# Optimization experiments

Hardware: AMD Instinct MI355X
Metric: run time of the kernel (lower is better)

## Reference

```python
import jax, jax.numpy as jnp
import numpy as np

D_MODEL = 192
NODE_NUM = 64
DEPTH = 2
ALPHA = 0.05
NUM_LAYERS = 2
LN_EPS = 1e-5


def _gcn(x, p):
    # x: [N, in_dim*D_MODEL]; faithful port of GCN.forward (eval mode)
    nv1, nv2, ws, bs, wm, bm, we, be, wl, bl, g, b = p
    N = x.shape[0]
    in_dim = x.shape[1] // D_MODEL
    adp = jax.nn.softmax(jax.nn.relu(nv1 @ nv2), axis=1)            # [V,V]
    adj = adp + jnp.eye(NODE_NUM, dtype=x.dtype)
    a = adj / adj.sum(1, keepdims=True)                              # row-normalized
    h0 = jax.lax.conv_general_dilated(
        x.reshape(N, in_dim, D_MODEL), ws, (1,), 'VALID',
        dimension_numbers=('NCH', 'OIH', 'NCH')) + bs[None, :, None]  # [N,C,V]
    h = h0
    outs = [h0]
    for _ in range(DEPTH):
        h = ALPHA * h0 + (1.0 - ALPHA) * jnp.einsum('ncw,vw->ncv', h, a)
        outs.append(h)
    ho = jnp.concatenate(outs, axis=1)                               # [N,(DEPTH+1)C,V]
    ho = jax.nn.gelu(jnp.einsum('ncv,oc->nov', ho, wm) + bm[None, :, None], approximate=False)
    ho = jnp.einsum('ncv,oc->nov', ho, we) + be[None, :, None]       # [N,6,V]
    ho = jnp.einsum('nov,dv->nod', ho, wl) + bl                      # [N,6,D]
    mu = ho.mean(-1, keepdims=True)
    var = ((ho - mu) ** 2).mean(-1, keepdims=True)                   # biased, like torch LN
    ho = (ho - mu) / jnp.sqrt(var + LN_EPS) * g + b
    return ho.reshape(N, 6 * D_MODEL)


def _encoder(inp4, flag, layer_params):
    x = jnp.transpose(inp4, (2, 0, 1, 3)) if flag == 1 else jnp.transpose(inp4, (1, 0, 2, 3))
    W, B, O, D = x.shape
    L = W + O - 1
    N = W * B
    # input_transfer: shift row r by r along the slice axis
    place = jax.vmap(lambda xr, r: jax.lax.dynamic_update_slice(
        jnp.zeros((B, L, D), x.dtype), xr, (0, r, 0)))
    a = place(x, jnp.arange(W)).reshape(N, L, D)
    layer0_output = None
    output_all = None
    rows_layers, cols_layers = [], []
    for layer in range(NUM_LAYERS):
        if layer >= 1:
            a = output_all  # eval mode: F.dropout is identity
            if layer == 1:
                layer0_output = a
        p = layer_params[layer]

        def step(carry, x_t, p=p):
            h_row, h_col = carry
            gate = _gcn(jnp.concatenate([h_row, h_col, x_t], axis=-1), p)  # [N,6D]
            sg = jax.nn.sigmoid(gate[:, :4 * D])
            tg = jnp.tanh(gate[:, 4 * D:])
            ug_r, og_r, ug_c, og_c = jnp.split(sg, 4, axis=-1)
            ig_r, ig_c = jnp.split(tg, 2, axis=-1)
            h_row = jnp.tanh((1.0 - ug_r) * h_row + ug_r * ig_r) * og_r
            h_col = jnp.tanh((1.0 - ug_c) * h_col + ug_c * ig_c) * og_c
            out_s = jnp.concatenate([h_row, h_col], axis=-1)
            # col hidden is saved pre-roll, rolled for next step
            return (h_row, jnp.roll(h_col, B, axis=0)), (out_s, h_row, h_col)

        init = (jnp.zeros((N, D), x.dtype), jnp.zeros((N, D), x.dtype))
        _, (outs, hrows, hcols) = jax.lax.scan(step, init, jnp.swapaxes(a, 0, 1))
        output_all = jnp.swapaxes(outs, 0, 1)                        # [N,L,2D]
        if layer >= 1:
            output_all = output_all + layer0_output
        # rows saved at slice s>=O-1 from block loc = s-O+1
        rows = hrows.reshape(L, W, B, D)[jnp.arange(O - 1, L), jnp.arange(W)]  # [W,B,D]
        # cols saved at slice s>=W-1 from last batch block
        cols = hcols[W - 1:, (W - 1) * B:, :]                        # [O,B,D]
        rows_layers.append(rows)
        cols_layers.append(cols)
    hidden_row_all = jnp.stack(rows_layers).transpose(2, 0, 1, 3)    # [B,layers,W,D]
    hidden_col_all = jnp.stack(cols_layers).transpose(2, 0, 1, 3)    # [B,layers,O,D]
    if flag == 1:
        return output_all, hidden_col_all, hidden_row_all
    return output_all, hidden_row_all, hidden_col_all


def setup_inputs() -> dict:
    key = jax.random.key(0)
    ks = jax.random.split(key, 20)
    idx = [0]
    def nxt():
        k = ks[idx[0]]
        idx[0] += 1
        return k
    B, W, O = 8, 24, 48
    K = D_MODEL - NODE_NUM + 1  # 129
    cc, sc, nd = 16, 32, 40
    d = {"input": jax.random.normal(nxt(), (B, W, O, D_MODEL), dtype=jnp.float32)}
    for li, in_dim in enumerate([3, 4]):
        d[f"nodevec1_{li}"] = jax.random.normal(nxt(), (NODE_NUM, nd), dtype=jnp.float32)
        d[f"nodevec2_{li}"] = jax.random.normal(nxt(), (nd, NODE_NUM), dtype=jnp.float32)
        d[f"w_start_{li}"] = jax.random.normal(nxt(), (cc, in_dim, K), dtype=jnp.float32) * 0.05
        d[f"b_start_{li}"] = jnp.zeros((cc,), jnp.float32)
        d[f"w_mlp_{li}"] = jax.random.normal(nxt(), (sc, (DEPTH + 1) * cc), dtype=jnp.float32) * 0.05
        d[f"b_mlp_{li}"] = jnp.zeros((sc,), jnp.float32)
        d[f"w_end_{li}"] = jax.random.normal(nxt(), (6, sc), dtype=jnp.float32) * 0.05
        d[f"b_end_{li}"] = jnp.zeros((6,), jnp.float32)
        d[f"w_lin_{li}"] = jax.random.normal(nxt(), (D_MODEL, NODE_NUM), dtype=jnp.float32) * 0.05
        d[f"b_lin_{li}"] = jnp.zeros((D_MODEL,), jnp.float32)
        d[f"gamma_{li}"] = jnp.ones((D_MODEL,), jnp.float32)
        d[f"beta_{li}"] = jnp.zeros((D_MODEL,), jnp.float32)
    d["flag"] = 0
    return d


def reference(input, nodevec1_0, nodevec2_0, w_start_0, b_start_0, w_mlp_0, b_mlp_0,
              w_end_0, b_end_0, w_lin_0, b_lin_0, gamma_0, beta_0,
              nodevec1_1, nodevec2_1, w_start_1, b_start_1, w_mlp_1, b_mlp_1,
              w_end_1, b_end_1, w_lin_1, b_lin_1, gamma_1, beta_1, flag):
    p0 = (nodevec1_0, nodevec2_0, w_start_0, b_start_0, w_mlp_0, b_mlp_0,
          w_end_0, b_end_0, w_lin_0, b_lin_0, gamma_0, beta_0)
    p1 = (nodevec1_1, nodevec2_1, w_start_1, b_start_1, w_mlp_1, b_mlp_1,
          w_end_1, b_end_1, w_lin_1, b_lin_1, gamma_1, beta_1)
    return _encoder(input, flag, (p0, p1))
```

## Files before the change

### kernel.cpp

```cpp
#include <hip/hip_runtime.h>
#include <hip/hip_bf16.h>

#define NT 512
typedef unsigned short u16;
typedef unsigned long long u64;

__device__ __forceinline__ u16 tobf(float x) {
  union { __hip_bfloat16 h; u16 u; } cv;
  cv.h = __float2bfloat16(x);
  return cv.u;
}
__device__ __forceinline__ float frombf(u16 u) {
  return __uint_as_float(((unsigned)u) << 16);
}
__device__ __forceinline__ float sigf(float x) {
  return __builtin_amdgcn_rcpf(1.f + __builtin_amdgcn_exp2f(-1.4426950408889634f * x));
}
__device__ __forceinline__ float tanh_fast(float x) {
  return 1.f - 2.f * __builtin_amdgcn_rcpf(1.f + __builtin_amdgcn_exp2f(2.8853900817779268f * x));
}
__device__ __forceinline__ void lds_fence() {
  asm volatile("s_waitcnt lgkmcnt(0)" ::: "memory");
  __builtin_amdgcn_sched_barrier(0);
}
__device__ __forceinline__ void bar_light() {
  asm volatile("s_waitcnt lgkmcnt(0)" ::: "memory");
  __builtin_amdgcn_s_barrier();
  asm volatile("" ::: "memory");
}

struct SeqArgs {
  const float* input;
  const float* nv1_0; const float* nv2_0; const float* nv1_1; const float* nv2_1;
  const float* w_start0; const float* b_start0; const float* w_mlp0; const float* b_mlp0;
  const float* w_end0;   const float* b_end0;   const float* w_lin0; const float* b_lin0;
  const float* gamma0;   const float* beta0;
  const float* w_start1; const float* b_start1; const float* w_mlp1; const float* b_mlp1;
  const float* w_end1;   const float* b_end1;   const float* w_lin1; const float* b_lin1;
  const float* gamma1;   const float* beta1;
  u64*   HCOL2;
  int*   prog;
  float* out_all; float* out_hrow; float* out_hcol;
};

__global__ __launch_bounds__(NT, 2) void seq_kernel(SeqArgs A) {
  const int n = blockIdx.x, w = n >> 3, b = n & 7, tid = threadIdx.x;
  const int pred = (n + 184) % 192;
  const int succ = (n + 8) % 192;

  __shared__ __align__(16) float sCIN[768];
  __shared__ __align__(16) u16   sWS[64 * 132];
  __shared__ __align__(16) float sAT[4096];
  __shared__ __align__(16) float sH[2][1024];
  __shared__ __align__(16) float sAbuf[4928];
  float* const sPart = sAbuf;
  float* const sG    = sAbuf;
  float* const sH2c  = sAbuf + 2048;
  float* const sE    = sAbuf + 2048;
  float* const sY    = sAbuf;
  float* const smWE  = sAbuf + 3072;
  float* const smBE  = sAbuf + 3264;
  float* const smWM  = sAbuf + 3328;

  for (int layer = 0; layer < 2; ++layer) {
    const int in_dim = 3 + layer;
    const int P = in_dim - 1;
    const float* nv1    = layer ? A.nv1_1    : A.nv1_0;
    const float* nv2    = layer ? A.nv2_1    : A.nv2_0;
    const float* wstart = layer ? A.w_start1 : A.w_start0;
    const float* bs     = layer ? A.b_start1 : A.b_start0;
    const float* wm     = layer ? A.w_mlp1   : A.w_mlp0;
    const float* bm     = layer ? A.b_mlp1   : A.b_mlp0;
    const float* we     = layer ? A.w_end1   : A.w_end0;
    const float* be     = layer ? A.b_end1   : A.b_end0;
    const float* wl     = layer ? A.w_lin1   : A.w_lin0;
    const float* bl     = layer ? A.b_lin1   : A.b_lin0;
    const float* gm     = layer ? A.gamma1   : A.gamma0;
    const float* bt     = layer ? A.beta1    : A.beta0;

    for (int idx = tid; idx < 4096; idx += NT) {
      int v = idx >> 6, ww = idx & 63;
      float s = 0.f;
      for (int j = 0; j < 40; ++j) s = fmaf(nv1[v*40 + j], nv2[j*64 + ww], s);
      sAbuf[idx] = fmaxf(s, 0.f);
    }
    __syncthreads();
    if (tid < 64) {
      const int v = tid;
      float m = -1e30f;
      for (int ww = 0; ww < 64; ++ww) m = fmaxf(m, sAbuf[v*64 + ww]);
      float s = 0.f;
      for (int ww = 0; ww < 64; ++ww) { float e = expf(sAbuf[v*64 + ww] - m); sAbuf[v*64 + ww] = e; s += e; }
      float inv = 1.f / s, rs = 1.f;
      for (int ww = 0; ww < 64; ++ww) rs += sAbuf[v*64 + ww] * inv;
      float irs = 1.f / rs;
      for (int ww = 0; ww < 64; ++ww) {
        float a = sAbuf[v*64 + ww] * inv + ((ww == v) ? 1.f : 0.f);
        sAT[ww*64 + v] = a * irs;
      }
    }
    __syncthreads();
    for (int idx = tid; idx < 16*in_dim*132; idx += NT) {
      int row = idx / 132, k = idx - row*132;
      sWS[idx] = (k < 129) ? tobf(wstart[((row & 15)*in_dim + (row >> 4))*129 + k]) : (u16)0;
    }
    for (int idx = tid; idx < 1536; idx += NT) { int o = idx/48, c = idx - o*48; smWM[o*50 + c] = wm[idx]; }
    for (int idx = tid; idx < 192; idx += NT) smWE[idx] = we[idx];
    if (tid < 6) smBE[tid] = be[tid];
    for (int d = tid; d < 384; d += NT) sCIN[d] = 0.f;

    const int v_p = tid & 63;
    const int o0  = tid >> 6;
    const float bmv0 = bm[o0], bmv1 = bm[o0 + 8], bmv2 = bm[o0 + 16], bmv3 = bm[o0 + 24];
    float blv = 0.f, gmv = 1.f, btv = 0.f;
    if (tid < 384) blv = bl[(tid >= 192) ? tid - 192 : tid];
    if (tid < 192) { gmv = gm[tid]; btv = bt[tid]; }
    float bs_r[2];
    bs_r[0] = bs[tid >> 6];
    bs_r[1] = bs[(tid >> 6) + 8];
    __syncthreads();

    auto pre_conv = [&]() {
      const int nslots = P << 8;
      for (int s = tid; s < nslots; s += NT) {
        const int cidx = s >> 4;
        const int p = cidx >> 4, c = cidx & 15;
        const int vg = s & 15;
        const int ich = (p == 0) ? 0 : (p + 1);
        const float* xin = ((p == 0) ? &sCIN[0] : &sCIN[384 + (p-1)*192]) + vg*4;
        const u16* wrow = &sWS[(ich*16 + c)*132];
        float a0 = 0.f, a1 = 0.f, a2 = 0.f, a3 = 0.f;
        float4 xc = *(const float4*)xin;
        for (int k4 = 0; k4 < 128; k4 += 4) {
          ushort4 wu = *(const ushort4*)(wrow + k4);
          float w0 = frombf(wu.x), w1 = frombf(wu.y), w2 = frombf(wu.z), w3 = frombf(wu.w);
          float4 xn = *(const float4*)(xin + k4 + 4);
          a0 = fmaf(w3, xc.w, fmaf(w2, xc.z, fmaf(w1, xc.y, fmaf(w0, xc.x, a0))));
          a1 = fmaf(w3, xn.x, fmaf(w2, xc.w, fmaf(w1, xc.z, fmaf(w0, xc.y, a1))));
          a2 = fmaf(w3, xn.y, fmaf(w2, xn.x, fmaf(w1, xc.w, fmaf(w0, xc.z, a2))));
          a3 = fmaf(w3, xn.z, fmaf(w2, xn.y, fmaf(w1, xn.x, fmaf(w0, xc.w, a3))));
          xc = xn;
        }
        float wk = frombf(wrow[128]);
        a0 = fmaf(wk, xc.x, a0); a1 = fmaf(wk, xc.y, a1);
        a2 = fmaf(wk, xc.z, a2); a3 = fmaf(wk, xc.w, a3);
        *(float4*)&sPart[cidx*64 + vg*4] = make_float4(a0, a1, a2, a3);
      }
      bar_light();
      {
        const int c0 = tid >> 6, v = tid & 63;
        float sum0 = bs_r[0], sum1 = bs_r[1];
        for (int p = 0; p < P; ++p) {
          sum0 += sPart[(p*16 + c0     )*64 + v];
          sum1 += sPart[(p*16 + c0 + 8 )*64 + v];
        }
        sH[0][ c0      *64 + v] = sum0;
        sH[0][(c0 + 8 )*64 + v] = sum1;
      }
      bar_light();
    };

    {
      if (layer == 0) {
        int o = 0 - w;
        if (o >= 0 && o < 48) {
          const float* xr = A.input + (((size_t)(b*24 + w)*48 + o)*192);
          for (int d = tid; d < 192; d += NT) sCIN[384 + d] = xr[d];
        } else {
          for (int d = tid; d < 192; d += NT) sCIN[384 + d] = 0.f;
        }
      } else {
        const float* xr = A.out_all + ((size_t)n*71 + 0)*384;
        for (int d = tid; d < 384; d += NT) sCIN[384 + d] = xr[d];
      }
      bar_light();
      pre_conv();
    }

    for (int t = 0; t < 71; ++t) {
      const int S = layer*71 + t;

      float xpa = 0.f, xpb = 0.f;
      if (t < 70 && tid < 192) {
        if (layer == 0) {
          int o = (t + 1) - w;
          if (o >= 0 && o < 48)
            xpa = A.input[(((size_t)(b*24 + w)*48 + o)*192) + tid];
        } else {
          const float* xr = A.out_all + ((size_t)n*71 + (t+1))*384;
          xpa = xr[tid];
          xpb = xr[192 + tid];
        }
      }

      if (t > 0) {
        if (tid < 192) {
          const u64* src = &A.HCOL2[((size_t)((S-1) & 15)*192 + pred)*192 + tid];
          u64 v;
          do {
            v = __hip_atomic_load(src, __ATOMIC_RELAXED, __HIP_MEMORY_SCOPE_AGENT);
          } while ((unsigned)(v >> 32) != (unsigned)S);
          sCIN[192 + tid] = __uint_as_float((unsigned)v);
        } else if (tid == 256 && S >= 16) {
          while (__hip_atomic_load(&A.prog[succ*32], __ATOMIC_RELAXED, __HIP_MEMORY_SCOPE_AGENT) < S - 15)
            __builtin_amdgcn_s_sleep(2);
        }
        bar_light();
        if (tid == 0)
          __hip_atomic_store(&A.prog[n*32], S, __ATOMIC_RELAXED, __HIP_MEMORY_SCOPE_AGENT);
      } else if (S >= 16) {
        if (tid == 256) {
          while (__hip_atomic_load(&A.prog[succ*32], __ATOMIC_RELAXED, __HIP_MEMORY_SCOPE_AGENT) < S - 15)
            __builtin_amdgcn_s_sleep(2);
        }
      }

      {
        const int c = tid >> 5, vg2 = tid & 31;
        const int vbase = c*64 + vg2*2;
        const float* xin = &sCIN[192 + vg2*2];
        const u16* wrow = &sWS[(16 + c)*132];
        float a0 = sH[0][vbase], a1 = sH[0][vbase + 1];
        float2 xc = *(const float2*)xin;
        for (int k2 = 0; k2 < 128; k2 += 2) {
          ushort2 wu = *(const ushort2*)(wrow + k2);
          float w0 = frombf(wu.x), w1 = frombf(wu.y);
          float2 xn = *(const float2*)(xin + k2 + 2);
          a0 = fmaf(w1, xc.y, fmaf(w0, xc.x, a0));
          a1 = fmaf(w1, xn.x, fmaf(w0, xc.y, a1));
          xc = xn;
        }
        float wk = frombf(wrow[128]);
        a0 = fmaf(wk, xc.x, a0); a1 = fmaf(wk, xc.y, a1);
        sH[0][vbase] = a0; sH[0][vbase + 1] = a1;
      }
      lds_fence();
      {
        const int c0 = o0 * 2;
        float pa0 = 0.f, pa1 = 0.f;
        for (int w4 = 0; w4 < 64; w4 += 4) {
          float a0v = sAT[(w4+0)*64 + v_p];
          float a1v = sAT[(w4+1)*64 + v_p];
          float a2v = sAT[(w4+2)*64 + v_p];
          float a3v = sAT[(w4+3)*64 + v_p];
          float4 h0v = *(const float4*)&sH[0][ c0      *64 + w4];
          float4 h1v = *(const float4*)&sH[0][(c0 + 1 )*64 + w4];
          pa0 = fmaf(h0v.x, a0v, pa0); pa0 = fmaf(h0v.y, a1v, pa0);
          pa0 = fmaf(h0v.z, a2v, pa0); pa0 = fmaf(h0v.w, a3v, pa0);
          pa1 = fmaf(h1v.x, a0v, pa1); pa1 = fmaf(h1v.y, a1v, pa1);
          pa1 = fmaf(h1v.z, a2v, pa1); pa1 = fmaf(h1v.w, a3v, pa1);
        }
        float h0a = sH[0][ c0      *64 + v_p];
        float h0b = sH[0][(c0 + 1 )*64 + v_p];
        sH[1][ c0      *64 + v_p] = fmaf(0.95f, pa0, 0.05f * h0a);
        sH[1][(c0 + 1 )*64 + v_p] = fmaf(0.95f, pa1, 0.05f * h0b);
        lds_fence();
        float pb0 = 0.f, pb1 = 0.f;
        for (int w4 = 0; w4 < 64; w4 += 4) {
          float a0v = sAT[(w4+0)*64 + v_p];
          float a1v = sAT[(w4+1)*64 + v_p];
          float a2v = sAT[(w4+2)*64 + v_p];
          float a3v = sAT[(w4+3)*64 + v_p];
          float4 h0v = *(const float4*)&sH[1][ c0      *64 + w4];
          float4 h1v = *(const float4*)&sH[1][(c0 + 1 )*64 + w4];
          pb0 = fmaf(h0v.x, a0v, pb0); pb0 = fmaf(h0v.y, a1v, pb0);
          pb0 = fmaf(h0v.z, a2v, pb0); pb0 = fmaf(h0v.w, a3v, pb0);
          pb1 = fmaf(h1v.x, a0v, pb1); pb1 = fmaf(h1v.y, a1v, pb1);
          pb1 = fmaf(h1v.z, a2v, pb1); pb1 = fmaf(h1v.w, a3v, pb1);
        }
        sH2c[ c0      *64 + v_p] = fmaf(0.95f, pb0, 0.05f * h0a);
        sH2c[(c0 + 1 )*64 + v_p] = fmaf(0.95f, pb1, 0.05f * h0b);
      }
      bar_light();

      {
        float g0 = bmv0, g1 = bmv1, g2 = bmv2, g3 = bmv3;
#pragma unroll
        for (int c = 0; c < 16; ++c) {
          float h0v = sH[0][c*64 + v_p];
          float h1v = sH[1][c*64 + v_p];
          float h2v = sH2c[c*64 + v_p];
          g0 = fmaf(smWM[(o0     )*50 + c], h0v, fmaf(smWM[(o0     )*50 + 16 + c], h1v, fmaf(smWM[(o0     )*50 + 32 + c], h2v, g0)));
          g1 = fmaf(smWM[(o0 +  8)*50 + c], h0v, fmaf(smWM[(o0 +  8)*50 + 16 + c], h1v, fmaf(smWM[(o0 +  8)*50 + 32 + c], h2v, g1)));
          g2 = fmaf(smWM[(o0 + 16)*50 + c], h0v, fmaf(smWM[(o0 + 16)*50 + 16 + c], h1v, fmaf(smWM[(o0 + 16)*50 + 32 + c], h2v, g2)));
          g3 = fmaf(smWM[(o0 + 24)*50 + c], h0v, fmaf(smWM[(o0 + 24)*50 + 16 + c], h1v, fmaf(smWM[(o0 + 24)*50 + 32 + c], h2v, g3)));
        }
        g0 = 0.5f * g0 * (1.f + erff(g0 * 0.70710678118654752f));
        g1 = 0.5f * g1 * (1.f + erff(g1 * 0.70710678118654752f));
        g2 = 0.5f * g2 * (1.f + erff(g2 * 0.70710678118654752f));
        g3 = 0.5f * g3 * (1.f + erff(g3 * 0.70710678118654752f));
        sG[(o0     )*64 + v_p] = g0;
        sG[(o0 +  8)*64 + v_p] = g1;
        sG[(o0 + 16)*64 + v_p] = g2;
        sG[(o0 + 24)*64 + v_p] = g3;
      }
      bar_light();

      for (int idx = tid; idx < 384; idx += NT) {
        int o2 = idx >> 6, v = idx & 63;
        float acc = smBE[o2];
        for (int c = 0; c < 32; ++c) acc = fmaf(smWE[o2*32 + c], sG[c*64 + v], acc);
        sE[idx] = acc;
      }
      bar_light();

      if (tid < 384) {
        const int d  = (tid >= 192) ? tid - 192 : tid;
        const int r0 = (tid >= 192) ? 3 : 0;
        const float4* wrow = (const float4*)(wl + d*64);
        float y0 = blv, y1 = blv, y2 = blv;
        for (int q = 0; q < 16; ++q) {
          float4 wv = wrow[q];
          float4 e0 = *(const float4*)&sE[(r0+0)*64 + q*4];
          float4 e1 = *(const float4*)&sE[(r0+1)*64 + q*4];
          float4 e2 = *(const float4*)&sE[(r0+2)*64 + q*4];
          y0 = fmaf(e0.x,wv.x, fmaf(e0.y,wv.y, fmaf(e0.z,wv.z, fmaf(e0.w,wv.w, y0))));
          y1 = fmaf(e1.x,wv.x, fmaf(e1.y,wv.y, fmaf(e1.z,wv.z, fmaf(e1.w,wv.w, y1))));
          y2 = fmaf(e2.x,wv.x, fmaf(e2.y,wv.y, fmaf(e2.z,wv.z, fmaf(e2.w,wv.w, y2))));
        }
        sY[(r0+0)*192 + d] = y0;
        sY[(r0+1)*192 + d] = y1;
        sY[(r0+2)*192 + d] = y2;
      }
      bar_light();

      if (tid < 192) {
        const int r = tid >> 5, l32 = tid & 31;
        float sm = 0.f, sq = 0.f;
#pragma unroll
        for (int m = 0; m < 6; ++m) {
          float v = sY[r*192 + l32 + 32*m];
          sm += v; sq = fmaf(v, v, sq);
        }
#pragma unroll
        for (int off = 16; off >= 1; off >>= 1) {
          sm += __shfl_xor(sm, off);
          sq += __shfl_xor(sq, off);
        }
        if (l32 == 0) {
          float mu = sm * (1.f/192.f);
          float var = sq * (1.f/192.f) - mu*mu;
          sH[1][r] = mu;
          sH[1][8 + r] = rsqrtf(fmaxf(var, 0.f) + 1e-5f);
        }
      }
      bar_light();

      float hcn = 0.f;
      if (tid < 192) {
        const int d = tid;
        float y2 = fmaf((sY[2*192+d] - sH[1][2]) * sH[1][10], gmv, btv);
        float y3 = fmaf((sY[3*192+d] - sH[1][3]) * sH[1][11], gmv, btv);
        float y5 = fmaf((sY[5*192+d] - sH[1][5]) * sH[1][13], gmv, btv);
        float ugc = sigf(y2), ogc = sigf(y3), igc = tanh_fast(y5);
        float hc = sCIN[192 + d];
        hcn = tanh_fast(fmaf(ugc, igc, (1.f - ugc)*hc)) * ogc;
        u64 pk = ((u64)(unsigned)(S + 1) << 32) | (u64)__float_as_uint(hcn);
        __hip_atomic_store(&A.HCOL2[((size_t)(S & 15)*192 + n)*192 + d], pk,
                           __ATOMIC_RELAXED, __HIP_MEMORY_SCOPE_AGENT);
      }
      if (tid < 192) {
        const int d = tid;
        float y0 = fmaf((sY[0*192+d] - sH[1][0]) * sH[1][8],  gmv, btv);
        float y1 = fmaf((sY[1*192+d] - sH[1][1]) * sH[1][9],  gmv, btv);
        float y4 = fmaf((sY[4*192+d] - sH[1][4]) * sH[1][12], gmv, btv);
        float ugr = sigf(y0), ogr = sigf(y1), igr = tanh_fast(y4);
        float hr = sCIN[d];
        float hrn = tanh_fast(fmaf(ugr, igr, (1.f - ugr)*hr)) * ogr;
        sCIN[d] = hrn;
        float* oa = A.out_all + ((size_t)n*71 + t)*384;
        if (layer == 0) { oa[d] = hrn; oa[192 + d] = hcn; }
        else           { oa[d] = hrn + sCIN[384 + d]; oa[192 + d] = hcn + sCIN[576 + d]; }
        if (t == 47 + w)
          A.out_hrow[(((size_t)b*2 + layer)*24 + w)*192 + d] = hrn;
        if (w == 23 && t >= 23)
          A.out_hcol[(((size_t)b*2 + layer)*48 + (t - 23))*192 + d] = hcn;
        if (t < 70) {
          sCIN[384 + d] = xpa;
          if (layer == 1) sCIN[576 + d] = xpb;
        }
      }
      bar_light();
      if (t < 70) pre_conv();
    }
    __syncthreads();
  }
}

extern "C" void kernel_launch(void* const* d_in, const int* in_sizes, int n_in,
                              void* d_out, int out_size, void* d_ws, size_t ws_size,
                              hipStream_t stream) {
  (void)in_sizes; (void)n_in; (void)out_size; (void)ws_size;
  char* ws = (char*)d_ws;
  int* prog  = (int*)ws;
  u64* HCOL2 = (u64*)(ws + 24576);

  hipMemsetAsync(ws, 0, 24576 + 4718592, stream);

  SeqArgs A;
  A.input    = (const float*)d_in[0];
  A.nv1_0    = (const float*)d_in[1];  A.nv2_0 = (const float*)d_in[2];
  A.w_start0 = (const float*)d_in[3];  A.b_start0 = (const float*)d_in[4];
  A.w_mlp0   = (const float*)d_in[5];  A.b_mlp0   = (const float*)d_in[6];
  A.w_end0   = (const float*)d_in[7];  A.b_end0   = (const float*)d_in[8];
  A.w_lin0   = (const float*)d_in[9];  A.b_lin0   = (const float*)d_in[10];
  A.gamma0   = (const float*)d_in[11]; A.beta0    = (const float*)d_in[12];
  A.nv1_1    = (const float*)d_in[13]; A.nv2_1 = (const float*)d_in[14];
  A.w_start1 = (const float*)d_in[15]; A.b_start1 = (const float*)d_in[16];
  A.w_mlp1   = (const float*)d_in[17]; A.b_mlp1   = (const float*)d_in[18];
  A.w_end1   = (const float*)d_in[19]; A.b_end1   = (const float*)d_in[20];
  A.w_lin1   = (const float*)d_in[21]; A.b_lin1   = (const float*)d_in[22];
  A.gamma1   = (const float*)d_in[23]; A.beta1    = (const float*)d_in[24];
  A.HCOL2 = HCOL2; A.prog = prog;
  A.out_all  = (float*)d_out;
  A.out_hrow = (float*)d_out + 5234688;
  A.out_hcol = (float*)d_out + 5308416;

  seq_kernel<<<192, NT, 0, stream>>>(A);
}
```

Baseline: 2.644 ms.

## Overlap next-step input convolution with row update and store weights as float

The start convolution over the next timestep's input channels is split off. Idle threads (192-447) compute it into a separate buffer while threads 0-191 do the row-state update, using a double-buffered input slot. Only the h_row channel convolution stays on the critical path. Start weights are also kept in LDS as float (values still rounded to bf16), which removes per-element conversion at the cost of more LDS, and the spin-wait on neighbour state now sleeps between polls. The extra LDS buffers may lower occupancy, and the added barriers add sync cost.

```diff
diff --git a/kernel.cpp b/kernel.cpp
--- a/kernel.cpp
+++ b/kernel.cpp
@@ -27,6 +27,24 @@
   asm volatile("s_waitcnt lgkmcnt(0)" ::: "memory");
   __builtin_amdgcn_s_barrier();
   asm volatile("" ::: "memory");
+}
+
+__device__ __forceinline__ void conv4(const float* __restrict__ wrow,
+                                      const float* __restrict__ xin,
+                                      float& a0, float& a1, float& a2, float& a3) {
+  float4 xc = *(const float4*)xin;
+  for (int k4 = 0; k4 < 128; k4 += 4) {
+    float4 wv = *(const float4*)(wrow + k4);
+    float4 xn = *(const float4*)(xin + k4 + 4);
+    a0 = fmaf(wv.w, xc.w, fmaf(wv.z, xc.z, fmaf(wv.y, xc.y, fmaf(wv.x, xc.x, a0))));
+    a1 = fmaf(wv.w, xn.x, fmaf(wv.z, xc.w, fmaf(wv.y, xc.z, fmaf(wv.x, xc.y, a1))));
+    a2 = fmaf(wv.w, xn.y, fmaf(wv.z, xn.x, fmaf(wv.y, xc.w, fmaf(wv.x, xc.z, a2))));
+    a3 = fmaf(wv.w, xn.z, fmaf(wv.z, xn.y, fmaf(wv.y, xn.x, fmaf(wv.x, xc.w, a3))));
+    xc = xn;
+  }
+  float wk = wrow[128];
+  a0 = fmaf(wk, xc.x, a0); a1 = fmaf(wk, xc.y, a1);
+  a2 = fmaf(wk, xc.z, a2); a3 = fmaf(wk, xc.w, a3);
 }
 
 struct SeqArgs {
@@ -48,10 +66,12 @@
   const int pred = (n + 184) % 192;
   const int succ = (n + 8) % 192;
 
-  __shared__ __align__(16) float sCIN[768];
-  __shared__ __align__(16) u16   sWS[64 * 132];
+  __shared__ __align__(16) float sCIN[384];
+  __shared__ __align__(16) float sXB[2][384];
+  __shared__ __align__(16) float sWSf[64 * 132];
   __shared__ __align__(16) float sAT[4096];
   __shared__ __align__(16) float sH[2][1024];
+  __shared__ __align__(16) float sPreP[2048];
   __shared__ __align__(16) float sAbuf[4928];
   float* const sPart = sAbuf;
   float* const sG    = sAbuf;
@@ -102,7 +122,7 @@
     __syncthreads();
     for (int idx = tid; idx < 16*in_dim*132; idx += NT) {
       int row = idx / 132, k = idx - row*132;
-      sWS[idx] = (k < 129) ? tobf(wstart[((row & 15)*in_dim + (row >> 4))*129 + k]) : (u16)0;
+      sWSf[idx] = (k < 129) ? frombf(tobf(wstart[((row & 15)*in_dim + (row >> 4))*129 + k])) : 0.f;
     }
     for (int idx = tid; idx < 1536; idx += NT) { int o = idx/48, c = idx - o*48; smWM[o*50 + c] = wm[idx]; }
     for (int idx = tid; idx < 192; idx += NT) smWE[idx] = we[idx];
@@ -120,88 +140,72 @@
     bs_r[1] = bs[(tid >> 6) + 8];
     __syncthreads();
 
-    auto pre_conv = [&]() {
+    {
+      if (layer == 0) {
+        int o = 0 - w;
+        for (int d = tid; d < 192; d += NT)
+          sXB[0][d] = (o >= 0 && o < 48) ? A.input[(((size_t)(b*24 + w)*48 + o)*192) + d] : 0.f;
+      } else {
+        for (int d = tid; d < 384; d += NT)
+          sXB[0][d] = A.out_all[((size_t)n*71 + 0)*384 + d];
+      }
+      bar_light();
       const int nslots = P << 8;
       for (int s = tid; s < nslots; s += NT) {
         const int cidx = s >> 4;
         const int p = cidx >> 4, c = cidx & 15;
         const int vg = s & 15;
         const int ich = (p == 0) ? 0 : (p + 1);
-        const float* xin = ((p == 0) ? &sCIN[0] : &sCIN[384 + (p-1)*192]) + vg*4;
-        const u16* wrow = &sWS[(ich*16 + c)*132];
+        const float* xin = ((p == 0) ? &sCIN[0] : &sXB[0][(p-1)*192]) + vg*4;
         float a0 = 0.f, a1 = 0.f, a2 = 0.f, a3 = 0.f;
-        float4 xc = *(const float4*)xin;
-        for (int k4 = 0; k4 < 128; k4 += 4) {
-          ushort4 wu = *(const ushort4*)(wrow + k4);
-          float w0 = frombf(wu.x), w1 = frombf(wu.y), w2 = frombf(wu.z), w3 = frombf(wu.w);
-          float4 xn = *(const float4*)(xin + k4 + 4);
-          a0 = fmaf(w3, xc.w, fmaf(w2, xc.z, fmaf(w1, xc.y, fmaf(w0, xc.x, a0))));
-          a1 = fmaf(w3, xn.x, fmaf(w2, xc.w, fmaf(w1, xc.z, fmaf(w0, xc.y, a1))));
-          a2 = fmaf(w3, xn.y, fmaf(w2, xn.x, fmaf(w1, xc.w, fmaf(w0, xc.z, a2))));
-          a3 = fmaf(w3, xn.z, fmaf(w2, xn.y, fmaf(w1, xn.x, fmaf(w0, xc.w, a3))));
-          xc = xn;
-        }
-        float wk = frombf(wrow[128]);
-        a0 = fmaf(wk, xc.x, a0); a1 = fmaf(wk, xc.y, a1);
-        a2 = fmaf(wk, xc.z, a2); a3 = fmaf(wk, xc.w, a3);
-        *(float4*)&sPart[cidx*64 + vg*4] = make_float4(a0, a1, a2, a3);
+        conv4(&sWSf[(ich*16 + c)*132], xin, a0, a1, a2, a3);
+        float* dst = (p == 0) ? &sPart[c*64 + vg*4] : &sPreP[(p-1)*1024 + c*64 + vg*4];
+        *(float4*)dst = make_float4(a0, a1, a2, a3);
       }
       bar_light();
       {
         const int c0 = tid >> 6, v = tid & 63;
         float sum0 = bs_r[0], sum1 = bs_r[1];
-        for (int p = 0; p < P; ++p) {
-          sum0 += sPart[(p*16 + c0     )*64 + v];
-          sum1 += sPart[(p*16 + c0 + 8 )*64 + v];
-        }
-        sH[0][ c0      *64 + v] = sum0;
-        sH[0][(c0 + 8 )*64 + v] = sum1;
-      }
-      bar_light();
-    };
-
-    {
-      if (layer == 0) {
-        int o = 0 - w;
-        if (o >= 0 && o < 48) {
-          const float* xr = A.input + (((size_t)(b*24 + w)*48 + o)*192);
-          for (int d = tid; d < 192; d += NT) sCIN[384 + d] = xr[d];
-        } else {
-          for (int d = tid; d < 192; d += NT) sCIN[384 + d] = 0.f;
-        }
-      } else {
-        const float* xr = A.out_all + ((size_t)n*71 + 0)*384;
-        for (int d = tid; d < 384; d += NT) sCIN[384 + d] = xr[d];
-      }
-      bar_light();
-      pre_conv();
+        sum0 += sPart[c0*64 + v];
+        sum1 += sPart[(c0+8)*64 + v];
+        for (int p = 1; p < P; ++p) {
+          sum0 += sPreP[(p-1)*1024 + c0*64 + v];
+          sum1 += sPreP[(p-1)*1024 + (c0+8)*64 + v];
+        }
+        sH[0][ c0     *64 + v] = sum0;
+        sH[0][(c0 + 8)*64 + v] = sum1;
+      }
+      bar_light();
     }
 
     for (int t = 0; t < 71; ++t) {
       const int S = layer*71 + t;
 
       float xpa = 0.f, xpb = 0.f;
-      if (t < 70 && tid < 192) {
+      if (t < 70 && tid >= 256 && tid < 448) {
+        const int d = tid - 256;
         if (layer == 0) {
           int o = (t + 1) - w;
           if (o >= 0 && o < 48)
-            xpa = A.input[(((size_t)(b*24 + w)*48 + o)*192) + tid];
+            xpa = A.input[(((size_t)(b*24 + w)*48 + o)*192) + d];
         } else {
           const float* xr = A.out_all + ((size_t)n*71 + (t+1))*384;
-          xpa = xr[tid];
-          xpb = xr[192 + tid];
-        }
-      }
-
+          xpa = xr[d];
+          xpb = xr[192 + d];
+        }
+      }
       if (t > 0) {
         if (tid < 192) {
           const u64* src = &A.HCOL2[((size_t)((S-1) & 15)*192 + pred)*192 + tid];
-          u64 v;
-          do {
+          u64 v = __hip_atomic_load(src, __ATOMIC_RELAXED, __HIP_MEMORY_SCOPE_AGENT);
+          while ((unsigned)(v >> 32) != (unsigned)S) {
+            __builtin_amdgcn_s_sleep(1);
             v = __hip_atomic_load(src, __ATOMIC_RELAXED, __HIP_MEMORY_SCOPE_AGENT);
-          } while ((unsigned)(v >> 32) != (unsigned)S);
+          }
+          __builtin_amdgcn_sched_barrier(0);
+          asm volatile("" ::: "memory");
           sCIN[192 + tid] = __uint_as_float((unsigned)v);
-        } else if (tid == 256 && S >= 16) {
+        } else if (tid == 448 && S >= 16) {
           while (__hip_atomic_load(&A.prog[succ*32], __ATOMIC_RELAXED, __HIP_MEMORY_SCOPE_AGENT) < S - 15)
             __builtin_amdgcn_s_sleep(2);
         }
@@ -209,7 +213,7 @@
         if (tid == 0)
           __hip_atomic_store(&A.prog[n*32], S, __ATOMIC_RELAXED, __HIP_MEMORY_SCOPE_AGENT);
       } else if (S >= 16) {
-        if (tid == 256) {
+        if (tid == 448) {
           while (__hip_atomic_load(&A.prog[succ*32], __ATOMIC_RELAXED, __HIP_MEMORY_SCOPE_AGENT) < S - 15)
             __builtin_amdgcn_s_sleep(2);
         }
@@ -219,18 +223,17 @@
         const int c = tid >> 5, vg2 = tid & 31;
         const int vbase = c*64 + vg2*2;
         const float* xin = &sCIN[192 + vg2*2];
-        const u16* wrow = &sWS[(16 + c)*132];
+        const float* wrow = &sWSf[(16 + c)*132];
         float a0 = sH[0][vbase], a1 = sH[0][vbase + 1];
         float2 xc = *(const float2*)xin;
         for (int k2 = 0; k2 < 128; k2 += 2) {
-          ushort2 wu = *(const ushort2*)(wrow + k2);
-          float w0 = frombf(wu.x), w1 = frombf(wu.y);
+          float2 wv = *(const float2*)(wrow + k2);
           float2 xn = *(const float2*)(xin + k2 + 2);
-          a0 = fmaf(w1, xc.y, fmaf(w0, xc.x, a0));
-          a1 = fmaf(w1, xn.x, fmaf(w0, xc.y, a1));
+          a0 = fmaf(wv.y, xc.y, fmaf(wv.x, xc.x, a0));
+          a1 = fmaf(wv.y, xn.x, fmaf(wv.x, xc.y, a1));
           xc = xn;
         }
-        float wk = frombf(wrow[128]);
+        float wk = wrow[128];
         a0 = fmaf(wk, xc.x, a0); a1 = fmaf(wk, xc.y, a1);
         sH[0][vbase] = a0; sH[0][vbase + 1] = a1;
       }
@@ -358,7 +361,14 @@
         u64 pk = ((u64)(unsigned)(S + 1) << 32) | (u64)__float_as_uint(hcn);
         __hip_atomic_store(&A.HCOL2[((size_t)(S & 15)*192 + n)*192 + d], pk,
                            __ATOMIC_RELAXED, __HIP_MEMORY_SCOPE_AGENT);
-      }
+      } else if (t < 70 && tid >= 256 && tid < 448) {
+        const int d = tid - 256;
+        float* xbn = &sXB[(t+1) & 1][0];
+        xbn[d] = xpa;
+        if (layer == 1) xbn[192 + d] = xpb;
+      }
+      bar_light();
+
       if (tid < 192) {
         const int d = tid;
         float y0 = fmaf((sY[0*192+d] - sH[1][0]) * sH[1][8],  gmv, btv);
@@ -370,18 +380,51 @@
         sCIN[d] = hrn;
         float* oa = A.out_all + ((size_t)n*71 + t)*384;
         if (layer == 0) { oa[d] = hrn; oa[192 + d] = hcn; }
-        else           { oa[d] = hrn + sCIN[384 + d]; oa[192 + d] = hcn + sCIN[576 + d]; }
+        else {
+          const float* xbt = &sXB[t & 1][0];
+          oa[d] = hrn + xbt[d]; oa[192 + d] = hcn + xbt[192 + d];
+        }
         if (t == 47 + w)
           A.out_hrow[(((size_t)b*2 + layer)*24 + w)*192 + d] = hrn;
         if (w == 23 && t >= 23)
           A.out_hcol[(((size_t)b*2 + layer)*48 + (t - 23))*192 + d] = hcn;
-        if (t < 70) {
-          sCIN[384 + d] = xpa;
-          if (layer == 1) sCIN[576 + d] = xpb;
-        }
-      }
-      bar_light();
-      if (t < 70) pre_conv();
+      } else if (t < 70 && tid >= 192 && tid < 448) {
+        const int sl = tid - 192;
+        const int nx = (P - 1) << 8;
+        const float* xbn = &sXB[(t+1) & 1][0];
+        for (int s = sl; s < nx; s += 256) {
+          const int p = 1 + (s >> 8);
+          const int c = (s >> 4) & 15, vg = s & 15;
+          const int ich = p + 1;
+          float a0 = 0.f, a1 = 0.f, a2 = 0.f, a3 = 0.f;
+          conv4(&sWSf[(ich*16 + c)*132], &xbn[(p-1)*192 + vg*4], a0, a1, a2, a3);
+          *(float4*)&sPreP[(p-1)*1024 + c*64 + vg*4] = make_float4(a0, a1, a2, a3);
+        }
+      }
+      bar_light();
+
+      if (t < 70) {
+        if (tid < 256) {
+          const int c = tid >> 4, vg = tid & 15;
+          float a0 = 0.f, a1 = 0.f, a2 = 0.f, a3 = 0.f;
+          conv4(&sWSf[c*132], &sCIN[vg*4], a0, a1, a2, a3);
+          *(float4*)&sPart[c*64 + vg*4] = make_float4(a0, a1, a2, a3);
+        }
+        bar_light();
+        {
+          const int c0 = tid >> 6, v = tid & 63;
+          float sum0 = bs_r[0], sum1 = bs_r[1];
+          sum0 += sPart[c0*64 + v];
+          sum1 += sPart[(c0+8)*64 + v];
+          for (int p = 1; p < P; ++p) {
+            sum0 += sPreP[(p-1)*1024 + c0*64 + v];
+            sum1 += sPreP[(p-1)*1024 + (c0+8)*64 + v];
+          }
+          sH[0][ c0     *64 + v] = sum0;
+          sH[0][(c0 + 8)*64 + v] = sum1;
+        }
+        bar_light();
+      }
     }
     __syncthreads();
   }
@@ -395,7 +438,7 @@
   int* prog  = (int*)ws;
   u64* HCOL2 = (u64*)(ws + 24576);
 
-  hipMemsetAsync(ws, 0, 24576 + 4718592, stream);
+  (void)hipMemsetAsync(ws, 0, 24576 + 4718592, stream);
 
   SeqArgs A;
   A.input    = (const float*)d_in[0];
```

New measurement: 2.672 ms. No clear change (+1.0%).

## Transpose GCN intermediates in LDS and read MLP/end weights from global

Applied to the files above, without the earlier changes.

Stores the adjacency and per-step hidden states (h0,h1,h2,gelu outputs) in node-major padded LDS layouts so the propagation, MLP and end projections can use float4 reads. The MLP and end weights are now read directly from global memory, which is uniform across a wave, instead of being staged in LDS. The start-conv step now uses 256 threads with 4 outputs each, and the spin-wait gains a short sleep. The intent is fewer LDS instructions and bank conflicts on the serial per-timestep critical path, at the cost of extra LDS space, transposed stores, and reliance on cache hits for the weights.

```diff
diff --git a/kernel.cpp b/kernel.cpp
--- a/kernel.cpp
+++ b/kernel.cpp
@@ -50,17 +50,17 @@
 
   __shared__ __align__(16) float sCIN[768];
   __shared__ __align__(16) u16   sWS[64 * 132];
-  __shared__ __align__(16) float sAT[4096];
+  __shared__ __align__(16) float sATt[64 * 68];
   __shared__ __align__(16) float sH[2][1024];
-  __shared__ __align__(16) float sAbuf[4928];
+  __shared__ __align__(16) float sHt[3 * 1280];
+  __shared__ __align__(16) float sGt[64 * 44];
+  __shared__ __align__(16) float sAbuf[4096];
   float* const sPart = sAbuf;
-  float* const sG    = sAbuf;
-  float* const sH2c  = sAbuf + 2048;
   float* const sE    = sAbuf + 2048;
   float* const sY    = sAbuf;
-  float* const smWE  = sAbuf + 3072;
-  float* const smBE  = sAbuf + 3264;
-  float* const smWM  = sAbuf + 3328;
+  float* const h0t   = sHt;
+  float* const h1t   = sHt + 1280;
+  float* const h2t   = sHt + 2560;
 
   for (int layer = 0; layer < 2; ++layer) {
     const int in_dim = 3 + layer;
@@ -96,7 +96,7 @@
       float irs = 1.f / rs;
       for (int ww = 0; ww < 64; ++ww) {
         float a = sAbuf[v*64 + ww] * inv + ((ww == v) ? 1.f : 0.f);
-        sAT[ww*64 + v] = a * irs;
+        sATt[v*68 + ww] = a * irs;
       }
     }
     __syncthreads();
@@ -104,16 +104,13 @@
       int row = idx / 132, k = idx - row*132;
       sWS[idx] = (k < 129) ? tobf(wstart[((row & 15)*in_dim + (row >> 4))*129 + k]) : (u16)0;
     }
-    for (int idx = tid; idx < 1536; idx += NT) { int o = idx/48, c = idx - o*48; smWM[o*50 + c] = wm[idx]; }
-    for (int idx = tid; idx < 192; idx += NT) smWE[idx] = we[idx];
-    if (tid < 6) smBE[tid] = be[tid];
     for (int d = tid; d < 384; d += NT) sCIN[d] = 0.f;
 
     const int v_p = tid & 63;
     const int o0  = tid >> 6;
     const float bmv0 = bm[o0], bmv1 = bm[o0 + 8], bmv2 = bm[o0 + 16], bmv3 = bm[o0 + 24];
-    float blv = 0.f, gmv = 1.f, btv = 0.f;
-    if (tid < 384) blv = bl[(tid >= 192) ? tid - 192 : tid];
+    float blv = 0.f, gmv = 1.f, btv = 0.f, bev = 0.f;
+    if (tid < 384) { blv = bl[(tid >= 192) ? tid - 192 : tid]; bev = be[tid >> 6]; }
     if (tid < 192) { gmv = gm[tid]; btv = bt[tid]; }
     float bs_r[2];
     bs_r[0] = bs[tid >> 6];
@@ -196,10 +193,13 @@
       if (t > 0) {
         if (tid < 192) {
           const u64* src = &A.HCOL2[((size_t)((S-1) & 15)*192 + pred)*192 + tid];
-          u64 v;
-          do {
+          u64 v = __hip_atomic_load(src, __ATOMIC_RELAXED, __HIP_MEMORY_SCOPE_AGENT);
+          while ((unsigned)(v >> 32) != (unsigned)S) {
+            __builtin_amdgcn_s_sleep(1);
             v = __hip_atomic_load(src, __ATOMIC_RELAXED, __HIP_MEMORY_SCOPE_AGENT);
-          } while ((unsigned)(v >> 32) != (unsigned)S);
+          }
+          __builtin_amdgcn_sched_barrier(0);
+          asm volatile("" ::: "memory");
           sCIN[192 + tid] = __uint_as_float((unsigned)v);
         } else if (tid == 256 && S >= 16) {
           while (__hip_atomic_load(&A.prog[succ*32], __ATOMIC_RELAXED, __HIP_MEMORY_SCOPE_AGENT) < S - 15)
@@ -215,92 +215,129 @@
         }
       }
 
-      {
-        const int c = tid >> 5, vg2 = tid & 31;
-        const int vbase = c*64 + vg2*2;
-        const float* xin = &sCIN[192 + vg2*2];
+      if (tid < 256) {
+        const int c = tid >> 4, vg = tid & 15;
+        float4 acc = *(const float4*)&sH[0][c*64 + vg*4];
+        float a0 = acc.x, a1 = acc.y, a2 = acc.z, a3 = acc.w;
         const u16* wrow = &sWS[(16 + c)*132];
-        float a0 = sH[0][vbase], a1 = sH[0][vbase + 1];
-        float2 xc = *(const float2*)xin;
-        for (int k2 = 0; k2 < 128; k2 += 2) {
-          ushort2 wu = *(const ushort2*)(wrow + k2);
-          float w0 = frombf(wu.x), w1 = frombf(wu.y);
-          float2 xn = *(const float2*)(xin + k2 + 2);
-          a0 = fmaf(w1, xc.y, fmaf(w0, xc.x, a0));
-          a1 = fmaf(w1, xn.x, fmaf(w0, xc.y, a1));
+        const float* xin = &sCIN[192 + vg*4];
+        float4 xc = *(const float4*)xin;
+        for (int k4 = 0; k4 < 128; k4 += 4) {
+          ushort4 wu = *(const ushort4*)(wrow + k4);
+          float w0 = frombf(wu.x), w1 = frombf(wu.y), w2 = frombf(wu.z), w3 = frombf(wu.w);
+          float4 xn = *(const float4*)(xin + k4 + 4);
+          a0 = fmaf(w3, xc.w, fmaf(w2, xc.z, fmaf(w1, xc.y, fmaf(w0, xc.x, a0))));
+          a1 = fmaf(w3, xn.x, fmaf(w2, xc.w, fmaf(w1, xc.z, fmaf(w0, xc.y, a1))));
+          a2 = fmaf(w3, xn.y, fmaf(w2, xn.x, fmaf(w1, xc.w, fmaf(w0, xc.z, a2))));
+          a3 = fmaf(w3, xn.z, fmaf(w2, xn.y, fmaf(w1, xn.x, fmaf(w0, xc.w, a3))));
           xc = xn;
         }
         float wk = frombf(wrow[128]);
         a0 = fmaf(wk, xc.x, a0); a1 = fmaf(wk, xc.y, a1);
-        sH[0][vbase] = a0; sH[0][vbase + 1] = a1;
-      }
-      lds_fence();
+        a2 = fmaf(wk, xc.z, a2); a3 = fmaf(wk, xc.w, a3);
+        *(float4*)&sH[0][c*64 + vg*4] = make_float4(a0, a1, a2, a3);
+        const int v0 = vg*4;
+        h0t[(v0    )*20 + c] = a0;
+        h0t[(v0 + 1)*20 + c] = a1;
+        h0t[(v0 + 2)*20 + c] = a2;
+        h0t[(v0 + 3)*20 + c] = a3;
+      }
+      bar_light();
+
       {
         const int c0 = o0 * 2;
         float pa0 = 0.f, pa1 = 0.f;
         for (int w4 = 0; w4 < 64; w4 += 4) {
-          float a0v = sAT[(w4+0)*64 + v_p];
-          float a1v = sAT[(w4+1)*64 + v_p];
-          float a2v = sAT[(w4+2)*64 + v_p];
-          float a3v = sAT[(w4+3)*64 + v_p];
+          float4 av = *(const float4*)&sATt[v_p*68 + w4];
           float4 h0v = *(const float4*)&sH[0][ c0      *64 + w4];
           float4 h1v = *(const float4*)&sH[0][(c0 + 1 )*64 + w4];
-          pa0 = fmaf(h0v.x, a0v, pa0); pa0 = fmaf(h0v.y, a1v, pa0);
-          pa0 = fmaf(h0v.z, a2v, pa0); pa0 = fmaf(h0v.w, a3v, pa0);
-          pa1 = fmaf(h1v.x, a0v, pa1); pa1 = fmaf(h1v.y, a1v, pa1);
-          pa1 = fmaf(h1v.z, a2v, pa1); pa1 = fmaf(h1v.w, a3v, pa1);
+          pa0 = fmaf(h0v.x, av.x, pa0); pa0 = fmaf(h0v.y, av.y, pa0);
+          pa0 = fmaf(h0v.z, av.z, pa0); pa0 = fmaf(h0v.w, av.w, pa0);
+          pa1 = fmaf(h1v.x, av.x, pa1); pa1 = fmaf(h1v.y, av.y, pa1);
+          pa1 = fmaf(h1v.z, av.z, pa1); pa1 = fmaf(h1v.w, av.w, pa1);
         }
         float h0a = sH[0][ c0      *64 + v_p];
         float h0b = sH[0][(c0 + 1 )*64 + v_p];
-        sH[1][ c0      *64 + v_p] = fmaf(0.95f, pa0, 0.05f * h0a);
-        sH[1][(c0 + 1 )*64 + v_p] = fmaf(0.95f, pa1, 0.05f * h0b);
+        float h1a = fmaf(0.95f, pa0, 0.05f * h0a);
+        float h1b = fmaf(0.95f, pa1, 0.05f * h0b);
+        sH[1][ c0      *64 + v_p] = h1a;
+        sH[1][(c0 + 1 )*64 + v_p] = h1b;
+        h1t[v_p*20 + c0    ] = h1a;
+        h1t[v_p*20 + c0 + 1] = h1b;
         lds_fence();
         float pb0 = 0.f, pb1 = 0.f;
         for (int w4 = 0; w4 < 64; w4 += 4) {
-          float a0v = sAT[(w4+0)*64 + v_p];
-          float a1v = sAT[(w4+1)*64 + v_p];
-          float a2v = sAT[(w4+2)*64 + v_p];
-          float a3v = sAT[(w4+3)*64 + v_p];
+          float4 av = *(const float4*)&sATt[v_p*68 + w4];
           float4 h0v = *(const float4*)&sH[1][ c0      *64 + w4];
           float4 h1v = *(const float4*)&sH[1][(c0 + 1 )*64 + w4];
-          pb0 = fmaf(h0v.x, a0v, pb0); pb0 = fmaf(h0v.y, a1v, pb0);
-          pb0 = fmaf(h0v.z, a2v, pb0); pb0 = fmaf(h0v.w, a3v, pb0);
-          pb1 = fmaf(h1v.x, a0v, pb1); pb1 = fmaf(h1v.y, a1v, pb1);
-          pb1 = fmaf(h1v.z, a2v, pb1); pb1 = fmaf(h1v.w, a3v, pb1);
-        }
-        sH2c[ c0      *64 + v_p] = fmaf(0.95f, pb0, 0.05f * h0a);
-        sH2c[(c0 + 1 )*64 + v_p] = fmaf(0.95f, pb1, 0.05f * h0b);
+          pb0 = fmaf(h0v.x, av.x, pb0); pb0 = fmaf(h0v.y, av.y, pb0);
+          pb0 = fmaf(h0v.z, av.z, pb0); pb0 = fmaf(h0v.w, av.w, pb0);
+          pb1 = fmaf(h1v.x, av.x, pb1); pb1 = fmaf(h1v.y, av.y, pb1);
+          pb1 = fmaf(h1v.z, av.z, pb1); pb1 = fmaf(h1v.w, av.w, pb1);
+        }
+        h2t[v_p*20 + c0    ] = fmaf(0.95f, pb0, 0.05f * h0a);
+        h2t[v_p*20 + c0 + 1] = fmaf(0.95f, pb1, 0.05f * h0b);
       }
       bar_light();
 
       {
         float g0 = bmv0, g1 = bmv1, g2 = bmv2, g3 = bmv3;
+        const float* wr0 = wm + (o0     )*48;
+        const float* wr1 = wm + (o0 +  8)*48;
+        const float* wr2 = wm + (o0 + 16)*48;
+        const float* wr3 = wm + (o0 + 24)*48;
+        for (int cq = 0; cq < 4; ++cq) {
+          float4 h0v = *(const float4*)&h0t[v_p*20 + cq*4];
+          float4 h1v = *(const float4*)&h1t[v_p*20 + cq*4];
+          float4 h2v = *(const float4*)&h2t[v_p*20 + cq*4];
+          float4 wa0 = *(const float4*)(wr0 + cq*4);
+          float4 wb0 = *(const float4*)(wr0 + 16 + cq*4);
+          float4 wc0 = *(const float4*)(wr0 + 32 + cq*4);
+          float4 wa1 = *(const float4*)(wr1 + cq*4);
+          float4 wb1 = *(const float4*)(wr1 + 16 + cq*4);
+          float4 wc1 = *(const float4*)(wr1 + 32 + cq*4);
+          float4 wa2 = *(const float4*)(wr2 + cq*4);
+          float4 wb2 = *(const float4*)(wr2 + 16 + cq*4);
+          float4 wc2 = *(const float4*)(wr2 + 32 + cq*4);
+          float4 wa3 = *(const float4*)(wr3 + cq*4);
+          float4 wb3 = *(const float4*)(wr3 + 16 + cq*4);
+          float4 wc3 = *(const float4*)(wr3 + 32 + cq*4);
+          const float* h0p = (const float*)&h0v;
+          const float* h1p = (const float*)&h1v;
+          const float* h2p = (const float*)&h2v;
 #pragma unroll
-        for (int c = 0; c < 16; ++c) {
-          float h0v = sH[0][c*64 + v_p];
-          float h1v = sH[1][c*64 + v_p];
-          float h2v = sH2c[c*64 + v_p];
-          g0 = fmaf(smWM[(o0     )*50 + c], h0v, fmaf(smWM[(o0     )*50 + 16 + c], h1v, fmaf(smWM[(o0     )*50 + 32 + c], h2v, g0)));
-          g1 = fmaf(smWM[(o0 +  8)*50 + c], h0v, fmaf(smWM[(o0 +  8)*50 + 16 + c], h1v, fmaf(smWM[(o0 +  8)*50 + 32 + c], h2v, g1)));
-          g2 = fmaf(smWM[(o0 + 16)*50 + c], h0v, fmaf(smWM[(o0 + 16)*50 + 16 + c], h1v, fmaf(smWM[(o0 + 16)*50 + 32 + c], h2v, g2)));
-          g3 = fmaf(smWM[(o0 + 24)*50 + c], h0v, fmaf(smWM[(o0 + 24)*50 + 16 + c], h1v, fmaf(smWM[(o0 + 24)*50 + 32 + c], h2v, g3)));
+          for (int j = 0; j < 4; ++j) {
+            float h0s = h0p[j], h1s = h1p[j], h2s = h2p[j];
+            g0 = fmaf(((const float*)&wa0)[j], h0s, fmaf(((const float*)&wb0)[j], h1s, fmaf(((const float*)&wc0)[j], h2s, g0)));
+            g1 = fmaf(((const float*)&wa1)[j], h0s, fmaf(((const float*)&wb1)[j], h1s, fmaf(((const float*)&wc1)[j], h2s, g1)));
+            g2 = fmaf(((const float*)&wa2)[j], h0s, fmaf(((const float*)&wb2)[j], h1s, fmaf(((const float*)&wc2)[j], h2s, g2)));
+            g3 = fmaf(((const float*)&wa3)[j], h0s, fmaf(((const float*)&wb3)[j], h1s, fmaf(((const float*)&wc3)[j], h2s, g3)));
+          }
         }
         g0 = 0.5f * g0 * (1.f + erff(g0 * 0.70710678118654752f));
         g1 = 0.5f * g1 * (1.f + erff(g1 * 0.70710678118654752f));
         g2 = 0.5f * g2 * (1.f + erff(g2 * 0.70710678118654752f));
         g3 = 0.5f * g3 * (1.f + erff(g3 * 0.70710678118654752f));
-        sG[(o0     )*64 + v_p] = g0;
-        sG[(o0 +  8)*64 + v_p] = g1;
-        sG[(o0 + 16)*64 + v_p] = g2;
-        sG[(o0 + 24)*64 + v_p] = g3;
-      }
-      bar_light();
-
-      for (int idx = tid; idx < 384; idx += NT) {
-        int o2 = idx >> 6, v = idx & 63;
-        float acc = smBE[o2];
-        for (int c = 0; c < 32; ++c) acc = fmaf(smWE[o2*32 + c], sG[c*64 + v], acc);
-        sE[idx] = acc;
+        sGt[v_p*44 + o0     ] = g0;
+        sGt[v_p*44 + o0 +  8] = g1;
+        sGt[v_p*44 + o0 + 16] = g2;
+        sGt[v_p*44 + o0 + 24] = g3;
+      }
+      bar_light();
+
+      if (tid < 384) {
+        const int o2 = tid >> 6, v = tid & 63;
+        float acc = bev;
+        const float* wer = we + o2*32;
+        for (int c4 = 0; c4 < 8; ++c4) {
+          float4 wev = *(const float4*)(wer + c4*4);
+          float4 gv  = *(const float4*)&sGt[v*44 + c4*4];
+          acc = fmaf(wev.x, gv.x, acc);
+          acc = fmaf(wev.y, gv.y, acc);
+          acc = fmaf(wev.z, gv.z, acc);
+          acc = fmaf(wev.w, gv.w, acc);
+        }
+        sE[tid] = acc;
       }
       bar_light();
 
@@ -395,7 +432,7 @@
   int* prog  = (int*)ws;
   u64* HCOL2 = (u64*)(ws + 24576);
 
-  hipMemsetAsync(ws, 0, 24576 + 4718592, stream);
+  (void)hipMemsetAsync(ws, 0, 24576 + 4718592, stream);
 
   SeqArgs A;
   A.input    = (const float*)d_in[0];
```

Measured after the change: 2.951 ms. 11.6% more time.
